# Performance work log

Measured on AMD Instinct MI355X. Metric: run time of the kernel, lower is better.

## Reference

```python
import jax, jax.numpy as jnp
import numpy as np

C_EXP = 8.0  # fixed gate sharpness from the module (self.c = 8.0)

def setup_inputs() -> dict:
    key = jax.random.key(0)
    k1, k2, k3, k4 = jax.random.split(key, 4)
    B, T, D = 8, 4096, 1024
    x = jax.random.normal(k1, (B, T, D), dtype=jnp.float32)
    W_r = jax.random.normal(k2, (D, D), dtype=jnp.float32) * (1.0 / np.sqrt(D))
    W_i = jax.random.normal(k3, (D, D), dtype=jnp.float32) * (1.0 / np.sqrt(D))
    lambd = jax.random.normal(k4, (D,), dtype=jnp.float32)
    return {"x": x, "W_r": W_r, "W_i": W_i, "lambd": lambd}

def reference(x, W_r, W_i, lambd):
    # Gates (nn.Linear with bias=False: y = x @ W.T)
    r = jax.nn.sigmoid(jnp.einsum('btd,ed->bte', x, W_r))
    i = jax.nn.sigmoid(jnp.einsum('btd,ed->bte', x, W_i))
    # a = sigmoid(lambd) ** (c * r), computed stably in log space
    log_a = C_EXP * r * jax.nn.log_sigmoid(lambd)  # [B,T,D], log_a <= 0
    a = jnp.exp(log_a)
    # input-normalized injection: sqrt(1 - a^2) * (i * x)
    b = jnp.sqrt(jnp.maximum(1.0 - jnp.exp(2.0 * log_a), 0.0)) * (i * x)
    # linear recurrence h_t = a_t * h_{t-1} + b_t via associative scan over T
    def combine(c1, c2):
        a1, b1 = c1
        a2, b2 = c2
        return (a1 * a2, a2 * b1 + b2)
    _, h = jax.lax.associative_scan(combine, (a, b), axis=1)
    return h
```

## Files before the change

kernel.cpp:

```cpp
#include <hip/hip_runtime.h>
#include <hip/hip_bf16.h>
#include <cstdint>

#define B_   8
#define T_   4096
#define D_   1024
#define M_   (B_*T_)
#define K_   D_
#define N_   D_

#define TC2  64
#define NC2  (T_/TC2)

#define BM   128
#define BN   128
#define BK   64

typedef __attribute__((ext_vector_type(8))) short  short8;
typedef __attribute__((ext_vector_type(4))) float  floatx4;

#define XB_OFF    0ull
#define WR_OFF    (XB_OFF + (size_t)M_*K_*2)
#define WI_OFF    (WR_OFF + (size_t)N_*K_*2)
#define LS_OFF    (WI_OFF + (size_t)N_*K_*2)
#define ASUM_OFF  (LS_OFF + (size_t)D_*4)
#define ESUM_OFF  (ASUM_OFF + (size_t)B_*NC2*D_*4)
#define WS_NEED   (ESUM_OFF + (size_t)B_*NC2*D_*4)

__device__ __forceinline__ uint32_t f2bf(float f) {
  uint32_t u = __float_as_uint(f);
  return (u + 0x7fffu + ((u >> 16) & 1u)) >> 16;
}

__device__ __forceinline__ void gload_lds16(const void* g, void* l) {
  __builtin_amdgcn_global_load_lds(
      (const __attribute__((address_space(1))) void*)g,
      (__attribute__((address_space(3))) void*)l, 16, 0, 0);
}

__global__ __launch_bounds__(256) void convert_kernel(
    const float* __restrict__ x, const float* __restrict__ wr,
    const float* __restrict__ wi, const float* __restrict__ lambd,
    uint2* __restrict__ xb, uint2* __restrict__ wrb, uint2* __restrict__ wib,
    float* __restrict__ ls) {
  int gid = blockIdx.x * 256 + threadIdx.x;
  if (gid < D_) {
    float l = lambd[gid];
    ls[gid] = fminf(l, 0.f) - log1pf(__expf(-fabsf(l)));
  }
  const int XQ = M_*K_/4;
  const int WQ = N_*K_/4;
  int stride = gridDim.x * 256;
  for (int q = gid; q < XQ + 2*WQ; q += stride) {
    const float4* src; uint2* dst; int i;
    if (q < XQ)           { src = (const float4*)x;  dst = xb;  i = q; }
    else if (q < XQ + WQ) { src = (const float4*)wr; dst = wrb; i = q - XQ; }
    else                  { src = (const float4*)wi; dst = wib; i = q - XQ - WQ; }
    float4 v = src[i];
    uint2 o;
    o.x = (f2bf(v.y) << 16) | f2bf(v.x);
    o.y = (f2bf(v.w) << 16) | f2bf(v.z);
    dst[i] = o;
  }
}

__global__ __launch_bounds__(256, 2) void dual_gemm_kernel(
    const short* __restrict__ xb, const short* __restrict__ wrb,
    const short* __restrict__ wib, const float* __restrict__ ls,
    uint32_t* __restrict__ ab, float* __restrict__ Asum,
    float* __restrict__ Esum) {
  __shared__ short lds[(BM + 2*BN) * BK];
  short* As  = lds;
  short* Brs = lds + BM*BK;
  short* Bis = lds + 2*BM*BK;

  const int tid  = threadIdx.x;
  const int lane = tid & 63;
  const int wv   = tid >> 6;
  const int wm   = wv >> 1;
  const int wn   = wv & 1;
  const int c16  = lane & 15;
  const int q    = lane >> 4;

  const int bm = blockIdx.x * BM;
  const int bn = blockIdx.y * BN;

  floatx4 accR[4][4], accI[4][4];
  #pragma unroll
  for (int i = 0; i < 4; ++i)
    #pragma unroll
    for (int j = 0; j < 4; ++j) {
      accR[i][j] = (floatx4){0.f,0.f,0.f,0.f};
      accI[i][j] = (floatx4){0.f,0.f,0.f,0.f};
    }

  const int srow0  = wv*32 + (lane >> 3);
  const int schunk = lane & 7;

  for (int k0 = 0; k0 < K_; k0 += BK) {
    #pragma unroll
    for (int l = 0; l < 4; ++l) {
      int r  = srow0 + l*8;
      int cc = schunk ^ (r & 7);
      size_t goff = (size_t)k0 + cc*8;
      gload_lds16(xb  + (size_t)(bm + r)*K_ + goff, As  + wv*2048 + l*512);
      gload_lds16(wrb + (size_t)(bn + r)*K_ + goff, Brs + wv*2048 + l*512);
      gload_lds16(wib + (size_t)(bn + r)*K_ + goff, Bis + wv*2048 + l*512);
    }
    __syncthreads();

    #pragma unroll
    for (int kk = 0; kk < BK/32; ++kk) {
      short8 af[4], brf[4], bif[4];
      #pragma unroll
      for (int f = 0; f < 4; ++f) {
        int m_loc = wm*64 + f*16 + c16;
        int cph   = (kk*4 + q) ^ (m_loc & 7);
        af[f]  = *(const short8*)(As  + m_loc*64 + cph*8);
        int n_loc = wn*64 + f*16 + c16;
        int cphn  = (kk*4 + q) ^ (n_loc & 7);
        brf[f] = *(const short8*)(Brs + n_loc*64 + cphn*8);
        bif[f] = *(const short8*)(Bis + n_loc*64 + cphn*8);
      }
      #pragma unroll
      for (int fm = 0; fm < 4; ++fm)
        #pragma unroll
        for (int fn = 0; fn < 4; ++fn) {
          accR[fm][fn] = __builtin_amdgcn_mfma_f32_16x16x32_bf16(
              af[fm], brf[fn], accR[fm][fn], 0, 0, 0);
          accI[fm][fn] = __builtin_amdgcn_mfma_f32_16x16x32_bf16(
              af[fm], bif[fn], accI[fm][fn], 0, 0, 0);
        }
    }
    __syncthreads();
  }

  const int b_idx = bm >> 12;
  const int c2    = ((bm & (T_-1)) >> 6) + wm;
  #pragma unroll
  for (int fn = 0; fn < 4; ++fn) {
    int col = bn + wn*64 + fn*16 + c16;
    float lsv = ls[col];
    float WA = 1.f, WE = 0.f;
    #pragma unroll
    for (int fm = 0; fm < 4; ++fm) {
      float SA = 1.f, SE = 0.f;
      #pragma unroll
      for (int j = 0; j < 4; ++j) {
        int row = bm + wm*64 + fm*16 + q*4 + j;
        float pr = accR[fm][fn][j];
        float pi = accI[fm][fn][j];
        float rg = 1.f / (1.f + __expf(-pr));
        float ig = 1.f / (1.f + __expf(-pi));
        float la = 8.f * rg * lsv;
        uint32_t xu = (uint32_t)(uint16_t)xb[(size_t)row*K_ + col];
        float xv = __uint_as_float(xu << 16);
        float a2 = __expf(2.f * la);
        float bb = sqrtf(fmaxf(1.f - a2, 0.f)) * ig * xv;
        uint32_t pk = (f2bf(bb) << 16) | f2bf(la);
        ab[(size_t)row*N_ + col] = pk;
        float av  = __expf(__uint_as_float(pk << 16));
        float bbr = __uint_as_float(pk & 0xffff0000u);
        SA *= av;
        SE = fmaf(av, SE, bbr);
      }
      #pragma unroll
      for (int s = 16; s <= 32; s <<= 1) {
        float OA = __shfl_xor(SA, s);
        float OE = __shfl_xor(SE, s);
        SE = (lane & s) ? fmaf(SA, OE, SE)
                        : fmaf(OA, SE, OE);
        SA *= OA;
      }
      WE = fmaf(SA, WE, SE);
      WA *= SA;
    }
    if (q == 0) {
      int o = (b_idx * NC2 + c2) * D_ + col;
      Asum[o] = WA;
      Esum[o] = WE;
    }
  }
}

__global__ __launch_bounds__(256) void scan_carry(
    float* __restrict__ Asum, const float* __restrict__ Esum) {
  int b = blockIdx.x >> 2;
  int d = ((blockIdx.x & 3) << 8) + threadIdx.x;
  float carry = 0.f;
  #pragma unroll 8
  for (int c = 0; c < NC2; ++c) {
    int o = (b*NC2 + c)*D_ + d;
    float A = Asum[o], E = Esum[o];
    Asum[o] = carry;
    carry = fmaf(A, carry, E);
  }
}

__global__ __launch_bounds__(256) void scan_final(
    uint32_t* __restrict__ out, const float* __restrict__ carry_buf) {
  int blk = blockIdx.x;
  int dg = blk & 1;
  int c  = (blk >> 1) & (NC2 - 1);
  int b  = blk >> 7;
  int d2 = (dg << 8) + threadIdx.x;

  const float2* cb = (const float2*)(carry_buf + (size_t)(b*NC2 + c)*D_);
  float2 hc = cb[d2];
  float h0 = hc.x, h1 = hc.y;

  uint2* p = (uint2*)(out + ((size_t)(b*T_ + c*TC2))*D_) + d2;
  #pragma unroll 4
  for (int t = 0; t < TC2; ++t) {
    size_t o = (size_t)t * (D_/2);
    uint2 v = p[o];
    float a0 = __expf(__uint_as_float(v.x << 16));
    h0 = fmaf(a0, h0, __uint_as_float(v.x & 0xffff0000u));
    float a1 = __expf(__uint_as_float(v.y << 16));
    h1 = fmaf(a1, h1, __uint_as_float(v.y & 0xffff0000u));
    uint2 ov; ov.x = __float_as_uint(h0); ov.y = __float_as_uint(h1);
    p[o] = ov;
  }
}

extern "C" void kernel_launch(void* const* d_in, const int* in_sizes, int n_in,
                              void* d_out, int out_size, void* d_ws, size_t ws_size,
                              hipStream_t stream) {
  (void)in_sizes; (void)n_in; (void)out_size;
  if (ws_size < WS_NEED) return;

  const float* x     = (const float*)d_in[0];
  const float* Wr    = (const float*)d_in[1];
  const float* Wi    = (const float*)d_in[2];
  const float* lambd = (const float*)d_in[3];

  char* ws = (char*)d_ws;
  short* xb   = (short*)(ws + XB_OFF);
  short* wrb  = (short*)(ws + WR_OFF);
  short* wib  = (short*)(ws + WI_OFF);
  float* ls   = (float*)(ws + LS_OFF);
  float* Asum = (float*)(ws + ASUM_OFF);
  float* Esum = (float*)(ws + ESUM_OFF);

  uint32_t* ab = (uint32_t*)d_out;

  convert_kernel<<<4096, 256, 0, stream>>>(x, Wr, Wi, lambd,
                                           (uint2*)xb, (uint2*)wrb, (uint2*)wib, ls);
  dual_gemm_kernel<<<dim3(M_/BM, N_/BN), 256, 0, stream>>>(xb, wrb, wib, ls, ab,
                                                           Asum, Esum);
  scan_carry<<<B_ * 4, 256, 0, stream>>>(Asum, Esum);
  scan_final<<<B_ * NC2 * 2, 256, 0, stream>>>(ab, Asum);
}
```

Before: 445.6 us.

## Double-buffer LDS in dual GEMM with 256-row tiles and 512 threads

Doubles the GEMM M tile to 256 rows and uses 8 waves per block, so each weight tile loaded into LDS is reused across twice as many x rows. Adds a two-stage LDS ping-pong so the global-to-LDS loads for the next K step are issued before the MFMAs on the current one, removing one barrier per step. Also raises wave priority around the MFMA block with s_setprio. The cost is a 128 KB LDS footprint, which limits each CU to one block and lowers occupancy.

```diff
diff --git a/kernel.cpp b/kernel.cpp
--- a/kernel.cpp
+++ b/kernel.cpp
@@ -12,9 +12,10 @@
 #define TC2  64
 #define NC2  (T_/TC2)
 
-#define BM   128
+#define BM   256
 #define BN   128
 #define BK   64
+#define NSTEP (K_/BK)
 
 typedef __attribute__((ext_vector_type(8))) short  short8;
 typedef __attribute__((ext_vector_type(4))) float  floatx4;
@@ -64,15 +65,12 @@
   }
 }
 
-__global__ __launch_bounds__(256, 2) void dual_gemm_kernel(
+__global__ __launch_bounds__(512, 2) void dual_gemm_kernel(
     const short* __restrict__ xb, const short* __restrict__ wrb,
     const short* __restrict__ wib, const float* __restrict__ ls,
     uint32_t* __restrict__ ab, float* __restrict__ Asum,
     float* __restrict__ Esum) {
-  __shared__ short lds[(BM + 2*BN) * BK];
-  short* As  = lds;
-  short* Brs = lds + BM*BK;
-  short* Bis = lds + 2*BM*BK;
+  __shared__ short lds[2 * 32768];
 
   const int tid  = threadIdx.x;
   const int lane = tid & 63;
@@ -94,20 +92,38 @@
       accI[i][j] = (floatx4){0.f,0.f,0.f,0.f};
     }
 
-  const int srow0  = wv*32 + (lane >> 3);
+  const int srow   = lane >> 3;
   const int schunk = lane & 7;
 
-  for (int k0 = 0; k0 < K_; k0 += BK) {
+  auto stage = [&](int buf, int k0) {
+    short* dst = lds + buf * 32768;
     #pragma unroll
     for (int l = 0; l < 4; ++l) {
-      int r  = srow0 + l*8;
+      int r  = wv*32 + l*8 + srow;
       int cc = schunk ^ (r & 7);
-      size_t goff = (size_t)k0 + cc*8;
-      gload_lds16(xb  + (size_t)(bm + r)*K_ + goff, As  + wv*2048 + l*512);
-      gload_lds16(wrb + (size_t)(bn + r)*K_ + goff, Brs + wv*2048 + l*512);
-      gload_lds16(wib + (size_t)(bn + r)*K_ + goff, Bis + wv*2048 + l*512);
-    }
-    __syncthreads();
+      gload_lds16(xb + (size_t)(bm + r)*K_ + k0 + cc*8,
+                  dst + wv*2048 + l*512);
+    }
+    #pragma unroll
+    for (int l = 0; l < 2; ++l) {
+      int r  = wv*16 + l*8 + srow;
+      int cc = schunk ^ (r & 7);
+      gload_lds16(wrb + (size_t)(bn + r)*K_ + k0 + cc*8,
+                  dst + 16384 + wv*1024 + l*512);
+      gload_lds16(wib + (size_t)(bn + r)*K_ + k0 + cc*8,
+                  dst + 24576 + wv*1024 + l*512);
+    }
+  };
+
+  stage(0, 0);
+  __syncthreads();
+
+  for (int step = 0; step < NSTEP; ++step) {
+    if (step + 1 < NSTEP) stage((step + 1) & 1, (step + 1) * BK);
+
+    const short* As  = lds + (step & 1) * 32768;
+    const short* Brs = As + 16384;
+    const short* Bis = As + 24576;
 
     #pragma unroll
     for (int kk = 0; kk < BK/32; ++kk) {
@@ -122,6 +138,7 @@
         brf[f] = *(const short8*)(Brs + n_loc*64 + cphn*8);
         bif[f] = *(const short8*)(Bis + n_loc*64 + cphn*8);
       }
+      __builtin_amdgcn_s_setprio(1);
       #pragma unroll
       for (int fm = 0; fm < 4; ++fm)
         #pragma unroll
@@ -131,6 +148,7 @@
           accI[fm][fn] = __builtin_amdgcn_mfma_f32_16x16x32_bf16(
               af[fm], bif[fn], accI[fm][fn], 0, 0, 0);
         }
+      __builtin_amdgcn_s_setprio(0);
     }
     __syncthreads();
   }
@@ -246,7 +264,7 @@
 
   convert_kernel<<<4096, 256, 0, stream>>>(x, Wr, Wi, lambd,
                                            (uint2*)xb, (uint2*)wrb, (uint2*)wib, ls);
-  dual_gemm_kernel<<<dim3(M_/BM, N_/BN), 256, 0, stream>>>(xb, wrb, wib, ls, ab,
+  dual_gemm_kernel<<<dim3(M_/BM, N_/BN), 512, 0, stream>>>(xb, wrb, wib, ls, ab,
                                                            Asum, Esum);
   scan_carry<<<B_ * 4, 256, 0, stream>>>(Asum, Esum);
   scan_final<<<B_ * NC2 * 2, 256, 0, stream>>>(ab, Asum);
```

New measurement: 439.6 us. Within noise of the previous version (-1.3%).
